# Kernel optimization log

Hardware: AMD Instinct MI355X
Metric: run time of the kernel (lower is better)

Reference implementation:

```python
import jax, jax.numpy as jnp
import numpy as np

EMBED_DIM = 1024
SCALE = float(np.sqrt(EMBED_DIM))


def setup_inputs() -> dict:
    key = jax.random.key(0)
    ks = jax.random.split(key, 4)
    B, S, D = 4, 2048, EMBED_DIM
    x = jax.random.normal(ks[0], (B, S, D), dtype=jnp.float32)
    # causal mask: 1 where attention allowed, 0 where blocked
    mask = jnp.tril(jnp.ones((S, S), dtype=jnp.int32))
    init = 1.0 / np.sqrt(D)
    Wq = jax.random.normal(ks[1], (D, D), dtype=jnp.float32) * init
    Wk = jax.random.normal(ks[2], (D, D), dtype=jnp.float32) * init
    Wv = jax.random.normal(ks[3], (D, D), dtype=jnp.float32) * init
    bq = jnp.zeros((D,), dtype=jnp.float32)
    bk = jnp.zeros((D,), dtype=jnp.float32)
    bv = jnp.zeros((D,), dtype=jnp.float32)
    return {"x": x, "mask": mask, "Wq": Wq, "bq": bq, "Wk": Wk, "bk": bk, "Wv": Wv, "bv": bv}


def reference(x, mask, Wq, bq, Wk, bk, Wv, bv):
    # Q, K, V projections (torch Linear: x @ W^T + b; here W stored as (D_in, D_out))
    q = x @ Wq + bq  # (B, S, D)
    k = x @ Wk + bk
    v = x @ Wv + bv
    # attention scores: Q K^T / sqrt(D)
    scores = jnp.einsum("bsd,btd->bst", q, k) / SCALE  # (B, S, S)
    scores = jnp.where(mask == 0, -jnp.inf, scores)
    attn = jax.nn.softmax(scores, axis=-1)
    # dropout disabled (inference / eval mode)
    out = jnp.einsum("bst,btd->bsd", attn, v)  # (B, S, D)
    return out
```

## Files before the change

### kernel.cpp

```cpp
#include <hip/hip_runtime.h>
#include <math.h>

#define DMODEL 1024
#define SEQ 2048
#define BATCH 4
#define SCALE_INV (1.0f/32.0f)

typedef unsigned short ushort_t;
typedef __attribute__((ext_vector_type(8))) short bf16x8;
typedef __attribute__((ext_vector_type(4))) float f32x4;

__device__ __forceinline__ ushort_t f2bf(float f) {
    unsigned int u = __float_as_uint(f);
    unsigned int rounding = 0x7FFFu + ((u >> 16) & 1u);
    return (ushort_t)((u + rounding) >> 16);
}

#define GLOAD16(SRC, DST) \
    __builtin_amdgcn_global_load_lds( \
        (const __attribute__((address_space(1))) void*)(SRC), \
        (__attribute__((address_space(3))) void*)(DST), 16, 0, 0)

__device__ __forceinline__ int xcd_swz(int bid, int nwg) {
    return (bid & 7) * (nwg >> 3) + (bid >> 3);
}

__device__ __forceinline__ void gemm_core_128(
    const ushort_t* __restrict__ A, int lda,
    const ushort_t* __restrict__ Bt, int ldb,
    int arow0, int brow0, int ksteps,
    ushort_t* As, ushort_t* Bs,
    f32x4 acc[4][4])
{
    const int tid = threadIdx.x;
    const int l   = tid & 63;
    const int w   = tid >> 6;
    const int wr  = w >> 1;
    const int wc  = w & 1;

    for (int s = 0; s < ksteps; ++s) {
        const int k0 = s * 32;
        #pragma unroll
        for (int i = 0; i < 2; ++i) {
            const int off = i * 4096 + w * 1024 + l * 16;
            const int row = off >> 6;
            const int ke  = (off & 63) >> 1;
            GLOAD16(A + (size_t)(arow0 + row) * lda + k0 + ke,
                    (char*)As + i * 4096 + w * 1024);
        }
        #pragma unroll
        for (int i = 0; i < 2; ++i) {
            const int off = i * 4096 + w * 1024 + l * 16;
            const int row = off >> 6;
            const int ke  = (off & 63) >> 1;
            GLOAD16(Bt + (size_t)(brow0 + row) * ldb + k0 + ke,
                    (char*)Bs + i * 4096 + w * 1024);
        }
        __syncthreads();

        bf16x8 a[4], b[4];
        #pragma unroll
        for (int m = 0; m < 4; ++m)
            a[m] = *(const bf16x8*)(As + (wr * 64 + m * 16 + (l & 15)) * 32 + (l >> 4) * 8);
        #pragma unroll
        for (int n = 0; n < 4; ++n)
            b[n] = *(const bf16x8*)(Bs + (wc * 64 + n * 16 + (l & 15)) * 32 + (l >> 4) * 8);
        #pragma unroll
        for (int m = 0; m < 4; ++m)
            #pragma unroll
            for (int n = 0; n < 4; ++n)
                acc[m][n] = __builtin_amdgcn_mfma_f32_16x16x32_bf16(a[m], b[n], acc[m][n], 0, 0, 0);
        __syncthreads();
    }
}

__global__ __launch_bounds__(256) void qkv_gemm_mfma(
    const ushort_t* __restrict__ x,
    const ushort_t* __restrict__ wt,
    const float* __restrict__ bq, const float* __restrict__ bk, const float* __restrict__ bv,
    ushort_t* __restrict__ q, ushort_t* __restrict__ k, ushort_t* __restrict__ vt)
{
    __shared__ __align__(16) ushort_t As[128 * 32];
    __shared__ __align__(16) ushort_t Bs[128 * 32];

    const int wg = xcd_swz(blockIdx.x, 8 * 64 * 3);
    const int z  = wg >> 9;
    const int r  = wg & 511;
    const int by = r >> 3;
    const int bx = r & 7;

    const ushort_t* Bt = wt + (size_t)z * DMODEL * DMODEL;
    const float* bias = (z == 0) ? bq : (z == 1) ? bk : bv;
    const float scale = (z == 0) ? SCALE_INV : 1.0f;

    const int arow0 = by * 128;
    const int brow0 = bx * 128;

    f32x4 acc[4][4];
    #pragma unroll
    for (int m = 0; m < 4; ++m)
        #pragma unroll
        for (int n = 0; n < 4; ++n)
            acc[m][n] = (f32x4)(0.f);

    gemm_core_128(x, DMODEL, Bt, DMODEL, arow0, brow0, DMODEL / 32, As, Bs, acc);

    const int l  = threadIdx.x & 63;
    const int w  = threadIdx.x >> 6;
    const int wr = w >> 1, wc = w & 1;

    if (z < 2) {
        ushort_t* out = (z == 0) ? q : k;
        #pragma unroll
        for (int n = 0; n < 4; ++n) {
            const int gcol = brow0 + wc * 64 + n * 16 + (l & 15);
            const float bb = bias[gcol];
            #pragma unroll
            for (int m = 0; m < 4; ++m) {
                #pragma unroll
                for (int j = 0; j < 4; ++j) {
                    const int grow = arow0 + wr * 64 + m * 16 + (l >> 4) * 4 + j;
                    out[(size_t)grow * DMODEL + gcol] = f2bf((acc[m][n][j] + bb) * scale);
                }
            }
        }
    } else {
        ushort_t* vtb = vt + (size_t)(arow0 >> 11) * DMODEL * SEQ;
        #pragma unroll
        for (int n = 0; n < 4; ++n) {
            const int gcol = brow0 + wc * 64 + n * 16 + (l & 15);
            const float bb = bias[gcol];
            #pragma unroll
            for (int m = 0; m < 4; ++m) {
                const int t0 = (arow0 & 2047) + wr * 64 + m * 16 + (l >> 4) * 4;
                ushort4 o;
                o.x = f2bf(acc[m][n][0] + bb);
                o.y = f2bf(acc[m][n][1] + bb);
                o.z = f2bf(acc[m][n][2] + bb);
                o.w = f2bf(acc[m][n][3] + bb);
                *(ushort4*)(vtb + (size_t)gcol * SEQ + t0) = o;
            }
        }
    }
}

__global__ __launch_bounds__(256) void qkt_gemm_mfma(
    const ushort_t* __restrict__ q, const ushort_t* __restrict__ k,
    float* __restrict__ scores)
{
    const int wg = xcd_swz(blockIdx.x, 16 * 16 * BATCH);
    const int b  = wg >> 8;
    const int r  = wg & 255;
    const int st = r >> 4;
    const int tt = r & 15;
    if (tt > st) return;

    __shared__ __align__(16) ushort_t As[128 * 32];
    __shared__ __align__(16) ushort_t Bs[128 * 32];

    const ushort_t* A  = q + (size_t)b * SEQ * DMODEL;
    const ushort_t* Bt = k + (size_t)b * SEQ * DMODEL;
    float* out = scores + (size_t)b * SEQ * SEQ;

    f32x4 acc[4][4];
    #pragma unroll
    for (int m = 0; m < 4; ++m)
        #pragma unroll
        for (int n = 0; n < 4; ++n)
            acc[m][n] = (f32x4)(0.f);

    gemm_core_128(A, DMODEL, Bt, DMODEL, st * 128, tt * 128, DMODEL / 32, As, Bs, acc);

    const int l  = threadIdx.x & 63;
    const int w  = threadIdx.x >> 6;
    const int wr = w >> 1, wc = w & 1;
    #pragma unroll
    for (int m = 0; m < 4; ++m) {
        #pragma unroll
        for (int n = 0; n < 4; ++n) {
            const int gcol = tt * 128 + wc * 64 + n * 16 + (l & 15);
            #pragma unroll
            for (int j = 0; j < 4; ++j) {
                const int grow = st * 128 + wr * 64 + m * 16 + (l >> 4) * 4 + j;
                out[(size_t)grow * SEQ + gcol] = acc[m][n][j];
            }
        }
    }
}

__global__ __launch_bounds__(512) void softmax_rows(float* __restrict__ scores)
{
    const int s = blockIdx.x;
    const int b = blockIdx.y;
    const int tid = threadIdx.x;

    float* row = scores + ((size_t)b * SEQ + s) * SEQ;
    ushort_t* prow = (ushort_t*)row;
    const int nt = s + 1;

    __shared__ float e_sh[SEQ];
    __shared__ float red[512];

    float lmax = -INFINITY;
    const int nt4 = nt >> 2;
    for (int i = tid; i < nt4; i += 512) {
        const float4 f = ((const float4*)row)[i];
        ((float4*)e_sh)[i] = f;
        lmax = fmaxf(lmax, fmaxf(fmaxf(f.x, f.y), fmaxf(f.z, f.w)));
    }
    for (int t = nt4 * 4 + tid; t < nt; t += 512) {
        const float xv = row[t];
        e_sh[t] = xv;
        lmax = fmaxf(lmax, xv);
    }
    red[tid] = lmax;
    __syncthreads();
    for (int off = 256; off > 0; off >>= 1) {
        if (tid < off) red[tid] = fmaxf(red[tid], red[tid + off]);
        __syncthreads();
    }
    const float mx = red[0];
    __syncthreads();

    float lsum = 0.f;
    for (int i = tid; i < nt4; i += 512) {
        float4 f = ((const float4*)e_sh)[i];
        f.x = __expf(f.x - mx); f.y = __expf(f.y - mx);
        f.z = __expf(f.z - mx); f.w = __expf(f.w - mx);
        ((float4*)e_sh)[i] = f;
        lsum += f.x + f.y + f.z + f.w;
    }
    for (int t = nt4 * 4 + tid; t < nt; t += 512) {
        const float e = __expf(e_sh[t] - mx);
        e_sh[t] = e;
        lsum += e;
    }
    red[tid] = lsum;
    __syncthreads();
    for (int off = 256; off > 0; off >>= 1) {
        if (tid < off) red[tid] += red[tid + off];
        __syncthreads();
    }
    const float inv = 1.0f / red[0];
    __syncthreads();

    const int tmax = ((s >> 7) + 1) << 7;
    for (int t4 = tid * 4; t4 < tmax; t4 += 2048) {
        ushort4 o;
        o.x = (t4     < nt) ? f2bf(e_sh[t4    ] * inv) : (ushort_t)0;
        o.y = (t4 + 1 < nt) ? f2bf(e_sh[t4 + 1] * inv) : (ushort_t)0;
        o.z = (t4 + 2 < nt) ? f2bf(e_sh[t4 + 2] * inv) : (ushort_t)0;
        o.w = (t4 + 3 < nt) ? f2bf(e_sh[t4 + 3] * inv) : (ushort_t)0;
        *(ushort4*)(prow + t4) = o;
    }
}

__global__ __launch_bounds__(256) void pv_gemm_mfma(
    const float* __restrict__ scoresP, const ushort_t* __restrict__ vt,
    float* __restrict__ outp)
{
    const int wg = xcd_swz(blockIdx.x, 8 * 16 * BATCH);
    const int b  = wg >> 7;
    const int r  = wg & 127;
    const int st = r >> 3;
    const int dt = r & 7;

    __shared__ __align__(16) ushort_t As[128 * 32];
    __shared__ __align__(16) ushort_t Bs[128 * 32];

    const ushort_t* A  = (const ushort_t*)(scoresP + (size_t)b * SEQ * SEQ);
    const ushort_t* Bt = vt + (size_t)b * DMODEL * SEQ;
    float* out = outp + (size_t)b * SEQ * DMODEL;

    f32x4 acc[4][4];
    #pragma unroll
    for (int m = 0; m < 4; ++m)
        #pragma unroll
        for (int n = 0; n < 4; ++n)
            acc[m][n] = (f32x4)(0.f);

    const int ksteps = (st + 1) * 4;
    gemm_core_128(A, 2 * SEQ, Bt, SEQ, st * 128, dt * 128, ksteps, As, Bs, acc);

    const int l  = threadIdx.x & 63;
    const int w  = threadIdx.x >> 6;
    const int wr = w >> 1, wc = w & 1;
    #pragma unroll
    for (int m = 0; m < 4; ++m) {
        #pragma unroll
        for (int n = 0; n < 4; ++n) {
            const int gcol = dt * 128 + wc * 64 + n * 16 + (l & 15);
            #pragma unroll
            for (int j = 0; j < 4; ++j) {
                const int grow = st * 128 + wr * 64 + m * 16 + (l >> 4) * 4 + j;
                out[(size_t)grow * DMODEL + gcol] = acc[m][n][j];
            }
        }
    }
}

__global__ __launch_bounds__(256) void prep_kernel(
    const float* __restrict__ x, ushort_t* __restrict__ x_bf,
    const float* __restrict__ Wq, const float* __restrict__ Wk, const float* __restrict__ Wv,
    ushort_t* __restrict__ wt)
{
    __shared__ float tile[32][33];
    const int bid = blockIdx.x;
    const int tid = threadIdx.x;

    if (bid < 8192) {
        const int i = bid * 256 + tid;
        const float4 f = *(const float4*)(x + (size_t)i * 4);
        ushort4 o;
        o.x = f2bf(f.x); o.y = f2bf(f.y); o.z = f2bf(f.z); o.w = f2bf(f.w);
        *(ushort4*)(x_bf + (size_t)i * 4) = o;
    } else {
        const int id = bid - 8192;
        const int z  = id >> 10;
        const int t  = id & 1023;
        const int k0 = (t & 31) * 32;
        const int n0 = (t >> 5) * 32;
        const float* W = (z == 0) ? Wq : (z == 1) ? Wk : Wv;
        ushort_t* wtd = wt + (size_t)z * DMODEL * DMODEL;
        const int x_ = tid & 31, y = tid >> 5;
        #pragma unroll
        for (int i = 0; i < 4; ++i)
            tile[y + i * 8][x_] = W[(size_t)(k0 + y + i * 8) * DMODEL + n0 + x_];
        __syncthreads();
        #pragma unroll
        for (int i = 0; i < 4; ++i)
            wtd[(size_t)(n0 + y + i * 8) * DMODEL + k0 + x_] = f2bf(tile[x_][y + i * 8]);
    }
}

__global__ __launch_bounds__(1024) void qkv_gemm_f32(
    const float* __restrict__ x,
    const float* __restrict__ Wq, const float* __restrict__ bq,
    const float* __restrict__ Wk, const float* __restrict__ bk,
    const float* __restrict__ Wv, const float* __restrict__ bv,
    float* __restrict__ q, float* __restrict__ k, float* __restrict__ v)
{
    const float* W; const float* bias; float* out;
    const int z = blockIdx.z;
    if (z == 0)      { W = Wq; bias = bq; out = q; }
    else if (z == 1) { W = Wk; bias = bk; out = k; }
    else             { W = Wv; bias = bv; out = v; }

    __shared__ float As[32][33];
    __shared__ float Bs[32][33];
    const int tx = threadIdx.x, ty = threadIdx.y;
    const int row = blockIdx.y * 32 + ty;
    const int col = blockIdx.x * 32 + tx;

    float acc = 0.f;
    for (int k0 = 0; k0 < DMODEL; k0 += 32) {
        As[ty][tx] = x[(size_t)row * DMODEL + k0 + tx];
        Bs[ty][tx] = W[(size_t)(k0 + ty) * DMODEL + col];
        __syncthreads();
        #pragma unroll
        for (int kk = 0; kk < 32; ++kk)
            acc += As[ty][kk] * Bs[kk][tx];
        __syncthreads();
    }
    out[(size_t)row * DMODEL + col] = acc + bias[col];
}

__global__ __launch_bounds__(256) void attn_f32(
    const float* __restrict__ q, const float* __restrict__ k,
    const float* __restrict__ v, float* __restrict__ out)
{
    const int s = blockIdx.x, b = blockIdx.y, tid = threadIdx.x;
    __shared__ float qs[DMODEL];
    __shared__ float sc[SEQ];
    __shared__ float red[256];
    const float* qrow = q + ((size_t)b * SEQ + s) * DMODEL;
    for (int d = tid; d < DMODEL; d += 256) qs[d] = qrow[d];
    __syncthreads();
    const float* kb = k + (size_t)b * SEQ * DMODEL;
    const int nt = s + 1;
    float lmax = -INFINITY;
    for (int t = tid; t < nt; t += 256) {
        const float* krow = kb + (size_t)t * DMODEL;
        float acc = 0.f;
        for (int d = 0; d < DMODEL; d += 4) {
            const float4 kv = *(const float4*)(krow + d);
            acc += qs[d] * kv.x + qs[d+1] * kv.y + qs[d+2] * kv.z + qs[d+3] * kv.w;
        }
        acc *= SCALE_INV; sc[t] = acc; lmax = fmaxf(lmax, acc);
    }
    red[tid] = lmax; __syncthreads();
    for (int off = 128; off > 0; off >>= 1) { if (tid < off) red[tid] = fmaxf(red[tid], red[tid+off]); __syncthreads(); }
    const float mx = red[0]; __syncthreads();
    float lsum = 0.f;
    for (int t = tid; t < nt; t += 256) { const float e = expf(sc[t]-mx); sc[t]=e; lsum+=e; }
    red[tid] = lsum; __syncthreads();
    for (int off = 128; off > 0; off >>= 1) { if (tid < off) red[tid] += red[tid+off]; __syncthreads(); }
    const float inv = 1.0f / red[0]; __syncthreads();
    const float* vb = v + (size_t)b * SEQ * DMODEL;
    float a0=0,a1=0,a2=0,a3=0;
    for (int t = 0; t < nt; ++t) {
        const float p = sc[t];
        const float* vrow = vb + (size_t)t * DMODEL;
        a0 += p*vrow[tid]; a1 += p*vrow[tid+256]; a2 += p*vrow[tid+512]; a3 += p*vrow[tid+768];
    }
    float* orow = out + ((size_t)b * SEQ + s) * DMODEL;
    orow[tid]=a0*inv; orow[tid+256]=a1*inv; orow[tid+512]=a2*inv; orow[tid+768]=a3*inv;
}

extern "C" void kernel_launch(void* const* d_in, const int* in_sizes, int n_in,
                              void* d_out, int out_size, void* d_ws, size_t ws_size,
                              hipStream_t stream)
{
    const float* x  = (const float*)d_in[0];
    const float* Wq = (const float*)d_in[2];
    const float* bq = (const float*)d_in[3];
    const float* Wk = (const float*)d_in[4];
    const float* bk = (const float*)d_in[5];
    const float* Wv = (const float*)d_in[6];
    const float* bv = (const float*)d_in[7];
    float* out = (float*)d_out;

    const size_t SZ_XBF   = (size_t)BATCH * SEQ * DMODEL * 2;
    const size_t SZ_WT    = 3 * (size_t)DMODEL * DMODEL * 2;
    const size_t SZ_QKV   = (size_t)BATCH * SEQ * DMODEL * 2;
    const size_t SZ_SC    = (size_t)BATCH * SEQ * SEQ * 4;
    const size_t NEED = SZ_XBF + SZ_WT + 3 * SZ_QKV + SZ_SC;

    if (ws_size >= NEED) {
        char* p = (char*)d_ws;
        ushort_t* x_bf = (ushort_t*)p;              p += SZ_XBF;
        ushort_t* wt   = (ushort_t*)p;              p += SZ_WT;
        ushort_t* q_bf = (ushort_t*)p;              p += SZ_QKV;
        ushort_t* k_bf = (ushort_t*)p;              p += SZ_QKV;
        ushort_t* vt   = (ushort_t*)p;              p += SZ_QKV;
        float*    sc   = (float*)p;

        hipLaunchKernelGGL(prep_kernel, dim3(8192 + 3072), dim3(256), 0, stream,
                           x, x_bf, Wq, Wk, Wv, wt);
        hipLaunchKernelGGL(qkv_gemm_mfma, dim3(8 * 64 * 3), dim3(256), 0, stream,
                           x_bf, wt, bq, bk, bv, q_bf, k_bf, vt);
        hipLaunchKernelGGL(qkt_gemm_mfma, dim3(16 * 16 * BATCH), dim3(256), 0, stream,
                           q_bf, k_bf, sc);
        hipLaunchKernelGGL(softmax_rows, dim3(SEQ, BATCH), dim3(512), 0, stream, sc);
        hipLaunchKernelGGL(pv_gemm_mfma, dim3(8 * 16 * BATCH), dim3(256), 0, stream,
                           sc, vt, out);
    } else {
        const size_t elems = (size_t)BATCH * SEQ * DMODEL;
        float* q = (float*)d_ws;
        float* k = q + elems;
        float* v = k + elems;
        hipLaunchKernelGGL(qkv_gemm_f32, dim3(DMODEL / 32, BATCH * SEQ / 32, 3), dim3(32, 32), 0, stream,
                           x, Wq, bq, Wk, bk, Wv, bv, q, k, v);
        hipLaunchKernelGGL(attn_f32, dim3(SEQ, BATCH), dim3(256), 0, stream, q, k, v, out);
    }
}
```

Baseline: 213.4 us.

## Fuse exp into QK^T GEMM, defer softmax normalization, widen K tile to 64

The separate softmax pass is removed. The QK^T kernel now exponentiates its scores directly, without subtracting the row max, and writes bf16 probabilities plus per-tile row partial sums. A small kernel combines the partials into reciprocal row sums, and the PV GEMM scales its output by them. The GEMM core's K step grows from 32 to 64, and the QK^T grid enumerates only lower-triangular tiles instead of launching and early-exiting the upper ones. This removes the fp32 score round trip through memory. Dropping the max subtraction risks overflow if scores are large, which holds here only because the scaled scores are small.

```diff
diff --git a/kernel.cpp b/kernel.cpp
--- a/kernel.cpp
+++ b/kernel.cpp
@@ -25,7 +25,7 @@
     return (bid & 7) * (nwg >> 3) + (bid >> 3);
 }
 
-__device__ __forceinline__ void gemm_core_128(
+__device__ __forceinline__ void gemm_core_bk64(
     const ushort_t* __restrict__ A, int lda,
     const ushort_t* __restrict__ Bt, int ldb,
     int arow0, int brow0, int ksteps,
@@ -37,39 +37,40 @@
     const int w   = tid >> 6;
     const int wr  = w >> 1;
     const int wc  = w & 1;
+    const int ke  = (l & 7) * 8;
+    const int rsub = w * 8 + (l >> 3);
 
     for (int s = 0; s < ksteps; ++s) {
-        const int k0 = s * 32;
-        #pragma unroll
-        for (int i = 0; i < 2; ++i) {
-            const int off = i * 4096 + w * 1024 + l * 16;
-            const int row = off >> 6;
-            const int ke  = (off & 63) >> 1;
+        const int k0 = s * 64;
+        #pragma unroll
+        for (int i = 0; i < 4; ++i) {
+            const int row = i * 32 + rsub;
             GLOAD16(A + (size_t)(arow0 + row) * lda + k0 + ke,
                     (char*)As + i * 4096 + w * 1024);
         }
         #pragma unroll
-        for (int i = 0; i < 2; ++i) {
-            const int off = i * 4096 + w * 1024 + l * 16;
-            const int row = off >> 6;
-            const int ke  = (off & 63) >> 1;
+        for (int i = 0; i < 4; ++i) {
+            const int row = i * 32 + rsub;
             GLOAD16(Bt + (size_t)(brow0 + row) * ldb + k0 + ke,
                     (char*)Bs + i * 4096 + w * 1024);
         }
         __syncthreads();
 
-        bf16x8 a[4], b[4];
-        #pragma unroll
-        for (int m = 0; m < 4; ++m)
-            a[m] = *(const bf16x8*)(As + (wr * 64 + m * 16 + (l & 15)) * 32 + (l >> 4) * 8);
-        #pragma unroll
-        for (int n = 0; n < 4; ++n)
-            b[n] = *(const bf16x8*)(Bs + (wc * 64 + n * 16 + (l & 15)) * 32 + (l >> 4) * 8);
-        #pragma unroll
-        for (int m = 0; m < 4; ++m)
+        #pragma unroll
+        for (int kk = 0; kk < 2; ++kk) {
+            bf16x8 a[4], b[4];
+            #pragma unroll
+            for (int m = 0; m < 4; ++m)
+                a[m] = *(const bf16x8*)(As + (wr * 64 + m * 16 + (l & 15)) * 64 + kk * 32 + (l >> 4) * 8);
             #pragma unroll
             for (int n = 0; n < 4; ++n)
-                acc[m][n] = __builtin_amdgcn_mfma_f32_16x16x32_bf16(a[m], b[n], acc[m][n], 0, 0, 0);
+                b[n] = *(const bf16x8*)(Bs + (wc * 64 + n * 16 + (l & 15)) * 64 + kk * 32 + (l >> 4) * 8);
+            #pragma unroll
+            for (int m = 0; m < 4; ++m)
+                #pragma unroll
+                for (int n = 0; n < 4; ++n)
+                    acc[m][n] = __builtin_amdgcn_mfma_f32_16x16x32_bf16(a[m], b[n], acc[m][n], 0, 0, 0);
+        }
         __syncthreads();
     }
 }
@@ -80,8 +81,8 @@
     const float* __restrict__ bq, const float* __restrict__ bk, const float* __restrict__ bv,
     ushort_t* __restrict__ q, ushort_t* __restrict__ k, ushort_t* __restrict__ vt)
 {
-    __shared__ __align__(16) ushort_t As[128 * 32];
-    __shared__ __align__(16) ushort_t Bs[128 * 32];
+    __shared__ __align__(16) ushort_t As[128 * 64];
+    __shared__ __align__(16) ushort_t Bs[128 * 64];
 
     const int wg = xcd_swz(blockIdx.x, 8 * 64 * 3);
     const int z  = wg >> 9;
@@ -103,7 +104,7 @@
         for (int n = 0; n < 4; ++n)
             acc[m][n] = (f32x4)(0.f);
 
-    gemm_core_128(x, DMODEL, Bt, DMODEL, arow0, brow0, DMODEL / 32, As, Bs, acc);
+    gemm_core_bk64(x, DMODEL, Bt, DMODEL, arow0, brow0, DMODEL / 64, As, Bs, acc);
 
     const int l  = threadIdx.x & 63;
     const int w  = threadIdx.x >> 6;
@@ -144,23 +145,23 @@
     }
 }
 
-__global__ __launch_bounds__(256) void qkt_gemm_mfma(
+__global__ __launch_bounds__(256) void qkt_exp_mfma(
     const ushort_t* __restrict__ q, const ushort_t* __restrict__ k,
-    float* __restrict__ scores)
-{
-    const int wg = xcd_swz(blockIdx.x, 16 * 16 * BATCH);
-    const int b  = wg >> 8;
-    const int r  = wg & 255;
-    const int st = r >> 4;
-    const int tt = r & 15;
-    if (tt > st) return;
-
-    __shared__ __align__(16) ushort_t As[128 * 32];
-    __shared__ __align__(16) ushort_t Bs[128 * 32];
+    ushort_t* __restrict__ P, float* __restrict__ partials)
+{
+    const int wg = xcd_swz(blockIdx.x, 544);
+    const int b  = wg / 136;
+    const int i  = wg - b * 136;
+    int st = (int)((sqrtf(8.f * (float)i + 1.f) - 1.f) * 0.5f);
+    if (st * (st + 1) / 2 > i) st--;
+    else if ((st + 1) * (st + 2) / 2 <= i) st++;
+    const int tt = i - st * (st + 1) / 2;
+
+    __shared__ __align__(16) ushort_t As[128 * 64];
+    __shared__ __align__(16) ushort_t Bs[128 * 64];
 
     const ushort_t* A  = q + (size_t)b * SEQ * DMODEL;
     const ushort_t* Bt = k + (size_t)b * SEQ * DMODEL;
-    float* out = scores + (size_t)b * SEQ * SEQ;
 
     f32x4 acc[4][4];
     #pragma unroll
@@ -169,7 +170,78 @@
         for (int n = 0; n < 4; ++n)
             acc[m][n] = (f32x4)(0.f);
 
-    gemm_core_128(A, DMODEL, Bt, DMODEL, st * 128, tt * 128, DMODEL / 32, As, Bs, acc);
+    gemm_core_bk64(A, DMODEL, Bt, DMODEL, st * 128, tt * 128, DMODEL / 64, As, Bs, acc);
+
+    const int l  = threadIdx.x & 63;
+    const int w  = threadIdx.x >> 6;
+    const int wr = w >> 1, wc = w & 1;
+    ushort_t* pb = P + (size_t)b * SEQ * SEQ;
+    float* part = partials + ((size_t)b * 32 + (size_t)(tt * 2 + wc)) * SEQ;
+    const bool diag = (st == tt);
+
+    #pragma unroll
+    for (int m = 0; m < 4; ++m) {
+        #pragma unroll
+        for (int j = 0; j < 4; ++j) {
+            const int grow = st * 128 + wr * 64 + m * 16 + (l >> 4) * 4 + j;
+            float rs = 0.f;
+            #pragma unroll
+            for (int n = 0; n < 4; ++n) {
+                const int gcol = tt * 128 + wc * 64 + n * 16 + (l & 15);
+                float e = 0.f;
+                if (!diag || gcol <= grow) e = __expf(acc[m][n][j]);
+                rs += e;
+                pb[(size_t)grow * SEQ + gcol] = f2bf(e);
+            }
+            rs += __shfl_xor(rs, 1);
+            rs += __shfl_xor(rs, 2);
+            rs += __shfl_xor(rs, 4);
+            rs += __shfl_xor(rs, 8);
+            if ((l & 15) == 0) part[grow] = rs;
+        }
+    }
+}
+
+__global__ __launch_bounds__(256) void combine_inv(
+    const float* __restrict__ partials, float* __restrict__ inv)
+{
+    const int idx = blockIdx.x * 256 + threadIdx.x;
+    const int b   = idx >> 11;
+    const int row = idx & 2047;
+    const int hmax = ((row >> 7) + 1) * 2;
+    float s = 0.f;
+    for (int h = 0; h < hmax; ++h)
+        s += partials[((size_t)b * 32 + h) * SEQ + row];
+    inv[idx] = 1.0f / s;
+}
+
+__global__ __launch_bounds__(256) void pv_gemm_mfma(
+    const ushort_t* __restrict__ P, const ushort_t* __restrict__ vt,
+    const float* __restrict__ inv, float* __restrict__ outp)
+{
+    const int wg = xcd_swz(blockIdx.x, 8 * 16 * BATCH);
+    const int b  = wg >> 7;
+    const int r  = wg & 127;
+    const int st = r >> 3;
+    const int dt = r & 7;
+
+    __shared__ __align__(16) ushort_t As[128 * 64];
+    __shared__ __align__(16) ushort_t Bs[128 * 64];
+
+    const ushort_t* A  = P + (size_t)b * SEQ * SEQ;
+    const ushort_t* Bt = vt + (size_t)b * DMODEL * SEQ;
+    float* out = outp + (size_t)b * SEQ * DMODEL;
+    const float* invb = inv + ((size_t)b << 11);
+
+    f32x4 acc[4][4];
+    #pragma unroll
+    for (int m = 0; m < 4; ++m)
+        #pragma unroll
+        for (int n = 0; n < 4; ++n)
+            acc[m][n] = (f32x4)(0.f);
+
+    const int ksteps = (st + 1) * 2;
+    gemm_core_bk64(A, SEQ, Bt, SEQ, st * 128, dt * 128, ksteps, As, Bs, acc);
 
     const int l  = threadIdx.x & 63;
     const int w  = threadIdx.x >> 6;
@@ -177,123 +249,13 @@
     #pragma unroll
     for (int m = 0; m < 4; ++m) {
         #pragma unroll
-        for (int n = 0; n < 4; ++n) {
-            const int gcol = tt * 128 + wc * 64 + n * 16 + (l & 15);
-            #pragma unroll
-            for (int j = 0; j < 4; ++j) {
-                const int grow = st * 128 + wr * 64 + m * 16 + (l >> 4) * 4 + j;
-                out[(size_t)grow * SEQ + gcol] = acc[m][n][j];
-            }
-        }
-    }
-}
-
-__global__ __launch_bounds__(512) void softmax_rows(float* __restrict__ scores)
-{
-    const int s = blockIdx.x;
-    const int b = blockIdx.y;
-    const int tid = threadIdx.x;
-
-    float* row = scores + ((size_t)b * SEQ + s) * SEQ;
-    ushort_t* prow = (ushort_t*)row;
-    const int nt = s + 1;
-
-    __shared__ float e_sh[SEQ];
-    __shared__ float red[512];
-
-    float lmax = -INFINITY;
-    const int nt4 = nt >> 2;
-    for (int i = tid; i < nt4; i += 512) {
-        const float4 f = ((const float4*)row)[i];
-        ((float4*)e_sh)[i] = f;
-        lmax = fmaxf(lmax, fmaxf(fmaxf(f.x, f.y), fmaxf(f.z, f.w)));
-    }
-    for (int t = nt4 * 4 + tid; t < nt; t += 512) {
-        const float xv = row[t];
-        e_sh[t] = xv;
-        lmax = fmaxf(lmax, xv);
-    }
-    red[tid] = lmax;
-    __syncthreads();
-    for (int off = 256; off > 0; off >>= 1) {
-        if (tid < off) red[tid] = fmaxf(red[tid], red[tid + off]);
-        __syncthreads();
-    }
-    const float mx = red[0];
-    __syncthreads();
-
-    float lsum = 0.f;
-    for (int i = tid; i < nt4; i += 512) {
-        float4 f = ((const float4*)e_sh)[i];
-        f.x = __expf(f.x - mx); f.y = __expf(f.y - mx);
-        f.z = __expf(f.z - mx); f.w = __expf(f.w - mx);
-        ((float4*)e_sh)[i] = f;
-        lsum += f.x + f.y + f.z + f.w;
-    }
-    for (int t = nt4 * 4 + tid; t < nt; t += 512) {
-        const float e = __expf(e_sh[t] - mx);
-        e_sh[t] = e;
-        lsum += e;
-    }
-    red[tid] = lsum;
-    __syncthreads();
-    for (int off = 256; off > 0; off >>= 1) {
-        if (tid < off) red[tid] += red[tid + off];
-        __syncthreads();
-    }
-    const float inv = 1.0f / red[0];
-    __syncthreads();
-
-    const int tmax = ((s >> 7) + 1) << 7;
-    for (int t4 = tid * 4; t4 < tmax; t4 += 2048) {
-        ushort4 o;
-        o.x = (t4     < nt) ? f2bf(e_sh[t4    ] * inv) : (ushort_t)0;
-        o.y = (t4 + 1 < nt) ? f2bf(e_sh[t4 + 1] * inv) : (ushort_t)0;
-        o.z = (t4 + 2 < nt) ? f2bf(e_sh[t4 + 2] * inv) : (ushort_t)0;
-        o.w = (t4 + 3 < nt) ? f2bf(e_sh[t4 + 3] * inv) : (ushort_t)0;
-        *(ushort4*)(prow + t4) = o;
-    }
-}
-
-__global__ __launch_bounds__(256) void pv_gemm_mfma(
-    const float* __restrict__ scoresP, const ushort_t* __restrict__ vt,
-    float* __restrict__ outp)
-{
-    const int wg = xcd_swz(blockIdx.x, 8 * 16 * BATCH);
-    const int b  = wg >> 7;
-    const int r  = wg & 127;
-    const int st = r >> 3;
-    const int dt = r & 7;
-
-    __shared__ __align__(16) ushort_t As[128 * 32];
-    __shared__ __align__(16) ushort_t Bs[128 * 32];
-
-    const ushort_t* A  = (const ushort_t*)(scoresP + (size_t)b * SEQ * SEQ);
-    const ushort_t* Bt = vt + (size_t)b * DMODEL * SEQ;
-    float* out = outp + (size_t)b * SEQ * DMODEL;
-
-    f32x4 acc[4][4];
-    #pragma unroll
-    for (int m = 0; m < 4; ++m)
-        #pragma unroll
-        for (int n = 0; n < 4; ++n)
-            acc[m][n] = (f32x4)(0.f);
-
-    const int ksteps = (st + 1) * 4;
-    gemm_core_128(A, 2 * SEQ, Bt, SEQ, st * 128, dt * 128, ksteps, As, Bs, acc);
-
-    const int l  = threadIdx.x & 63;
-    const int w  = threadIdx.x >> 6;
-    const int wr = w >> 1, wc = w & 1;
-    #pragma unroll
-    for (int m = 0; m < 4; ++m) {
-        #pragma unroll
-        for (int n = 0; n < 4; ++n) {
-            const int gcol = dt * 128 + wc * 64 + n * 16 + (l & 15);
-            #pragma unroll
-            for (int j = 0; j < 4; ++j) {
-                const int grow = st * 128 + wr * 64 + m * 16 + (l >> 4) * 4 + j;
-                out[(size_t)grow * DMODEL + gcol] = acc[m][n][j];
+        for (int j = 0; j < 4; ++j) {
+            const int grow = st * 128 + wr * 64 + m * 16 + (l >> 4) * 4 + j;
+            const float iv = invb[grow];
+            #pragma unroll
+            for (int n = 0; n < 4; ++n) {
+                const int gcol = dt * 128 + wc * 64 + n * 16 + (l & 15);
+                out[(size_t)grow * DMODEL + gcol] = acc[m][n][j] * iv;
             }
         }
     }
@@ -420,11 +382,13 @@
     const float* bv = (const float*)d_in[7];
     float* out = (float*)d_out;
 
-    const size_t SZ_XBF   = (size_t)BATCH * SEQ * DMODEL * 2;
-    const size_t SZ_WT    = 3 * (size_t)DMODEL * DMODEL * 2;
-    const size_t SZ_QKV   = (size_t)BATCH * SEQ * DMODEL * 2;
-    const size_t SZ_SC    = (size_t)BATCH * SEQ * SEQ * 4;
-    const size_t NEED = SZ_XBF + SZ_WT + 3 * SZ_QKV + SZ_SC;
+    const size_t SZ_XBF  = (size_t)BATCH * SEQ * DMODEL * 2;
+    const size_t SZ_WT   = 3 * (size_t)DMODEL * DMODEL * 2;
+    const size_t SZ_QKV  = (size_t)BATCH * SEQ * DMODEL * 2;
+    const size_t SZ_P    = (size_t)BATCH * SEQ * SEQ * 2;
+    const size_t SZ_PART = (size_t)BATCH * 32 * SEQ * 4;
+    const size_t SZ_INV  = (size_t)BATCH * SEQ * 4;
+    const size_t NEED = SZ_XBF + SZ_WT + 3 * SZ_QKV + SZ_P + SZ_PART + SZ_INV;
 
     if (ws_size >= NEED) {
         char* p = (char*)d_ws;
@@ -433,17 +397,19 @@
         ushort_t* q_bf = (ushort_t*)p;              p += SZ_QKV;
         ushort_t* k_bf = (ushort_t*)p;              p += SZ_QKV;
         ushort_t* vt   = (ushort_t*)p;              p += SZ_QKV;
-        float*    sc   = (float*)p;
+        ushort_t* Pb   = (ushort_t*)p;              p += SZ_P;
+        float*    part = (float*)p;                 p += SZ_PART;
+        float*    inv  = (float*)p;
 
         hipLaunchKernelGGL(prep_kernel, dim3(8192 + 3072), dim3(256), 0, stream,
                            x, x_bf, Wq, Wk, Wv, wt);
         hipLaunchKernelGGL(qkv_gemm_mfma, dim3(8 * 64 * 3), dim3(256), 0, stream,
                            x_bf, wt, bq, bk, bv, q_bf, k_bf, vt);
-        hipLaunchKernelGGL(qkt_gemm_mfma, dim3(16 * 16 * BATCH), dim3(256), 0, stream,
-                           q_bf, k_bf, sc);
-        hipLaunchKernelGGL(softmax_rows, dim3(SEQ, BATCH), dim3(512), 0, stream, sc);
+        hipLaunchKernelGGL(qkt_exp_mfma, dim3(544), dim3(256), 0, stream,
+                           q_bf, k_bf, Pb, part);
+        hipLaunchKernelGGL(combine_inv, dim3(32), dim3(256), 0, stream, part, inv);
         hipLaunchKernelGGL(pv_gemm_mfma, dim3(8 * 16 * BATCH), dim3(256), 0, stream,
-                           sc, vt, out);
+                           Pb, vt, inv, out);
     } else {
         const size_t elems = (size_t)BATCH * SEQ * DMODEL;
         float* q = (float*)d_ws;
```

Result: faster. 202.9 us (-4.9%).
